# Kernel tuning notes

Measured on AMD Instinct MI355X. Metric: run time of the kernel, lower is better.

## Reference

```python
import jax, jax.numpy as jnp
import numpy as np

EPS = 1e-6  # flax GroupNorm default


def group_norm(x, scale, bias, num_groups):
    B, H, W, C = x.shape
    xg = x.reshape(B, H, W, num_groups, C // num_groups)
    mean = jnp.mean(xg, axis=(1, 2, 4), keepdims=True)
    var = jnp.var(xg, axis=(1, 2, 4), keepdims=True)
    xg = (xg - mean) * jax.lax.rsqrt(var + EPS)
    return xg.reshape(B, H, W, C) * scale + bias


def nin(h, w, b):
    # 1x1 conv / per-pixel dense: bhwc,cd->bhwd
    return jnp.einsum('bhwc,cd->bhwd', h, w) + b


def setup_inputs() -> dict:
    key = jax.random.key(0)
    ks = jax.random.split(key, 8)
    B, H, W, C = 16, 64, 64, 128
    s = 1.0 / np.sqrt(C)
    return {
        'x': jax.random.normal(ks[0], (B, H, W, C), jnp.float32),
        'gn_scale': jnp.ones((C,), jnp.float32),
        'gn_bias': jnp.zeros((C,), jnp.float32),
        'wq': jax.random.normal(ks[1], (C, C), jnp.float32) * s,
        'bq': jnp.zeros((C,), jnp.float32),
        'wk': jax.random.normal(ks[2], (C, C), jnp.float32) * s,
        'bk': jnp.zeros((C,), jnp.float32),
        'wv': jax.random.normal(ks[3], (C, C), jnp.float32) * s,
        'bv': jnp.zeros((C,), jnp.float32),
        'wo': jax.random.normal(ks[4], (C, C), jnp.float32) * s,
        'bo': jnp.zeros((C,), jnp.float32),
    }


def reference(x, gn_scale, gn_bias, wq, bq, wk, bk, wv, bv, wo, bo):
    B, H, W, C = x.shape
    num_groups = min(C // 4, 32)
    h = group_norm(x, gn_scale, gn_bias, num_groups)
    q = nin(h, wq, bq)
    k = nin(h, wk, bk)
    v = nin(h, wv, bv)
    # dense spatial attention; logits (B,H,W,H*W) materialized as in original
    w = jnp.einsum('bhwc,bHWc->bhwHW', q, k) * (C ** -0.5)
    w = w.reshape(B, H, W, H * W)
    w = jax.nn.softmax(w, axis=-1)
    w = w.reshape(B, H, W, H, W)
    h = jnp.einsum('bhwHW,bHWc->bhwc', w, v)
    h = nin(h, wo, bo)
    return x + h  # skip_rescale=False
```

## Files before the change

### kernel.cpp

```cpp
#include <hip/hip_runtime.h>
#include <hip/hip_bf16.h>

typedef unsigned short ushort_t;
typedef unsigned int uint_t;
typedef __attribute__((ext_vector_type(8))) short bf16x8;
typedef __attribute__((ext_vector_type(4))) float f32x4;

#define MFMA32(a, b, c) __builtin_amdgcn_mfma_f32_16x16x32_bf16(a, b, c, 0, 0, 0)

static constexpr int BATCH = 16;
static constexpr int SEQ   = 4096;
static constexpr int CH    = 128;
static constexpr int NGRP  = 32;
static constexpr float EPS = 1e-6f;
static constexpr float C2 = 0.08838834764831845f * 1.4426950408889634f;

__device__ inline ushort_t f2bf(float f) {
    uint_t u = __float_as_uint(f);
    u = (u + 0x7fff + ((u >> 16) & 1)) >> 16;
    return (ushort_t)u;
}

__device__ inline float exp2_fast(float x) {
    return __builtin_amdgcn_exp2f(x);
}

__global__ __launch_bounds__(256) void gn_wprep(const float* __restrict__ x,
                                                float* __restrict__ stats,
                                                const float* __restrict__ W0,
                                                const float* __restrict__ W1,
                                                const float* __restrict__ W2,
                                                const float* __restrict__ W3,
                                                ushort_t* __restrict__ wt) {
    int bid = blockIdx.x;
    int t = threadIdx.x;
    if (bid >= 256) {
        int m = bid - 256;
        const float* Ws[4] = {W0, W1, W2, W3};
        const float* W = Ws[m];
        ushort_t* out = wt + (size_t)m * CH * CH;
        __shared__ ushort_t tile[128][130];
        for (int i = 0; i < 16; ++i) {
            int idx = (t + i * 256) * 4;
            int kk = idx >> 7, n = idx & 127;
            float4 w4 = *(const float4*)(W + (size_t)kk * CH + n);
            tile[n + 0][kk] = f2bf(w4.x);
            tile[n + 1][kk] = f2bf(w4.y);
            tile[n + 2][kk] = f2bf(w4.z);
            tile[n + 3][kk] = f2bf(w4.w);
        }
        __syncthreads();
        for (int i = 0; i < 8; ++i) {
            int idx = (t + i * 256) * 8;
            int n = idx >> 7, kk = idx & 127;
            ushort_t tmp[8];
            for (int u = 0; u < 8; ++u) tmp[u] = tile[n][kk + u];
            *(uint4*)&out[(size_t)n * CH + kk] = *(const uint4*)tmp;
        }
        return;
    }
    int b = bid >> 4, chunk = bid & 15;
    int c4 = (t & 31) * 4;
    int rowoff = t >> 5;
    const float* xb = x + (size_t)b * SEQ * CH;
    float s1 = 0.f, s2 = 0.f;
    int base_row = chunk * 256;
    for (int i = 0; i < 32; ++i) {
        int r = base_row + i * 8 + rowoff;
        float4 v = *(const float4*)(xb + (size_t)r * CH + c4);
        s1 += v.x + v.y + v.z + v.w;
        s2 += v.x * v.x + v.y * v.y + v.z * v.z + v.w * v.w;
    }
    __shared__ float red[256][2];
    red[t][0] = s1; red[t][1] = s2;
    __syncthreads();
    if (t < 32) {
        float a1 = 0.f, a2 = 0.f;
        for (int ro = 0; ro < 8; ++ro) {
            a1 += red[ro * 32 + t][0];
            a2 += red[ro * 32 + t][1];
        }
        float* slot = stats + ((size_t)(b * 16 + chunk) * 32 + t) * 2;
        slot[0] = a1;
        slot[1] = a2;
    }
}

__global__ __launch_bounds__(512) void gemm_qkv(const float* __restrict__ x,
                                                const float* __restrict__ stats,
                                                const float* __restrict__ gsc,
                                                const float* __restrict__ gbi,
                                                const ushort_t* __restrict__ wt,
                                                const float* __restrict__ Bq,
                                                const float* __restrict__ Bk,
                                                const float* __restrict__ Bv,
                                                ushort_t* __restrict__ outq,
                                                ushort_t* __restrict__ outk,
                                                ushort_t* __restrict__ outvt) {
    __shared__ ushort_t lds_a[128][136];
    __shared__ float2 gstat[32];
    int t = threadIdx.x;
    int wv = t >> 6, lane = t & 63, quad = lane >> 4, l16 = lane & 15;
    size_t m0 = (size_t)blockIdx.x * 128;
    int batch = (int)(m0 >> 12);
    int seq0  = (int)(m0 & 4095);
    if (t < 32) {
        float sum = 0.f, sq = 0.f;
        for (int c = 0; c < 16; ++c) {
            const float* slot = stats + ((size_t)(batch * 16 + c) * 32 + t) * 2;
            sum += slot[0];
            sq  += slot[1];
        }
        float mean = sum / 16384.f;
        float var  = sq / 16384.f - mean * mean;
        gstat[t] = float2{mean, __frsqrt_rn(var + EPS)};
    }
    __syncthreads();
    for (int i = 0; i < 4; ++i) {
        int idx = (t + i * 512) * 8;
        int r = idx >> 7, c = idx & 127;
        size_t row = m0 + r;
        float4 xa = *(const float4*)(x + row * CH + c);
        float4 xc = *(const float4*)(x + row * CH + c + 4);
        float2 stA = gstat[c >> 2];
        float2 stB = gstat[(c >> 2) + 1];
        float4 sA = *(const float4*)(gsc + c), sB = *(const float4*)(gsc + c + 4);
        float4 bA = *(const float4*)(gbi + c), bB = *(const float4*)(gbi + c + 4);
        ushort_t tmp[8];
        tmp[0] = f2bf((xa.x - stA.x) * stA.y * sA.x + bA.x);
        tmp[1] = f2bf((xa.y - stA.x) * stA.y * sA.y + bA.y);
        tmp[2] = f2bf((xa.z - stA.x) * stA.y * sA.z + bA.z);
        tmp[3] = f2bf((xa.w - stA.x) * stA.y * sA.w + bA.w);
        tmp[4] = f2bf((xc.x - stB.x) * stB.y * sB.x + bB.x);
        tmp[5] = f2bf((xc.y - stB.x) * stB.y * sB.y + bB.y);
        tmp[6] = f2bf((xc.z - stB.x) * stB.y * sB.z + bB.z);
        tmp[7] = f2bf((xc.w - stB.x) * stB.y * sB.w + bB.w);
        *(uint4*)&lds_a[r][c] = *(const uint4*)tmp;
    }
    __syncthreads();
    for (int j = 0; j < 3; ++j) {
        const ushort_t* wtj = wt + (size_t)j * CH * CH;
        const float* Bi = (j == 0) ? Bq : (j == 1) ? Bk : Bv;
        f32x4 acc[8] = {};
        for (int kh = 0; kh < 2; ++kh) {
            int k0 = kh * 64;
            for (int ks = 0; ks < 2; ++ks) {
                bf16x8 afrag = *(const bf16x8*)&lds_a[wv * 16 + l16][k0 + ks * 32 + quad * 8];
                for (int tc = 0; tc < 8; ++tc) {
                    bf16x8 bfrag = *(const bf16x8*)(wtj + (size_t)(tc * 16 + l16) * CH + k0 + ks * 32 + quad * 8);
                    acc[tc] = MFMA32(afrag, bfrag, acc[tc]);
                }
            }
        }
        int rl = wv * 16 + quad * 4;
        for (int tc = 0; tc < 8; ++tc) {
            int col = tc * 16 + l16;
            float bval = Bi[col];
            if (j == 2) {
                ushort_t tmp[4];
                for (int r = 0; r < 4; ++r) tmp[r] = f2bf(acc[tc][r] + bval);
                *(uint2*)&outvt[(size_t)batch * CH * SEQ + (size_t)col * SEQ + seq0 + rl] =
                    *(const uint2*)tmp;
            } else {
                ushort_t* op = (j == 0) ? outq : outk;
                for (int r = 0; r < 4; ++r) {
                    float vv = acc[tc][r] + bval;
                    if (j == 0) vv *= C2;
                    op[(m0 + rl + r) * CH + col] = f2bf(vv);
                }
            }
        }
    }
}

__global__ __launch_bounds__(256, 2) void flash_attn18(const ushort_t* __restrict__ q,
                                                       const ushort_t* __restrict__ k,
                                                       const ushort_t* __restrict__ vt,
                                                       ushort_t* __restrict__ o) {
    int bid = blockIdx.x;
    int b = bid & 15, qt = bid >> 4;
    int t = threadIdx.x;
    int wv = t >> 6, lane = t & 63, quad = lane >> 4, l16 = lane & 15;
    const size_t SB = (size_t)SEQ * CH;
    const ushort_t* qb  = q  + (size_t)b * SB;
    const ushort_t* kb  = k  + (size_t)b * SB;
    const ushort_t* vtb = vt + (size_t)b * SB;

    __shared__ ushort_t lds_k[2][64][136];
    __shared__ ushort_t lds_vt[2][128][72];

    int qrow_base = qt * 128 + wv * 32;
    bf16x8 qfrag[2][4];
#pragma unroll
    for (int nt = 0; nt < 2; ++nt)
#pragma unroll
        for (int ks = 0; ks < 4; ++ks)
            qfrag[nt][ks] = *(const bf16x8*)(qb + (size_t)(qrow_base + nt * 16 + l16) * CH + ks * 32 + quad * 8);

    f32x4 oacc[8][2] = {};
    float psum[2] = {0.f, 0.f};

    int kr_row  = t >> 4;
    int kr_col  = (t & 15) * 8;
    int vr_d    = t >> 3;
    int vr_beta = t & 7;
    int vc0 = 32 * (vr_beta >> 2) + 16 * (vr_beta & 1) + 4 * ((vr_beta >> 1) & 1);

    const ushort_t* kp = kb + (size_t)kr_row * CH + kr_col;
    const ushort_t* vp = vtb + (size_t)vr_d * SEQ + vr_beta * 8;

    uint4 kr[4], vr[4], k1[4];
#pragma unroll
    for (int i = 0; i < 4; ++i) kr[i] = *(const uint4*)(kp + (size_t)i * 16 * CH);
#pragma unroll
    for (int i = 0; i < 4; ++i) vr[i] = *(const uint4*)(vp + (size_t)i * 32 * SEQ);
#pragma unroll
    for (int i = 0; i < 4; ++i) k1[i] = *(const uint4*)(kp + (size_t)(64 + i * 16) * CH);
    kp += 2 * 64 * CH;
    vp += 64;
#pragma unroll
    for (int i = 0; i < 4; ++i) {
        *(uint4*)&lds_k[0][kr_row + 16 * i][kr_col] = kr[i];
        *(uint4*)&lds_k[1][kr_row + 16 * i][kr_col] = k1[i];
        *(uint2*)&lds_vt[0][vr_d + 32 * i][vc0]     = uint2{vr[i].x, vr[i].y};
        *(uint2*)&lds_vt[0][vr_d + 32 * i][vc0 + 8] = uint2{vr[i].z, vr[i].w};
    }
    __syncthreads();

    bf16x8 pkp[2][2];
    {
        f32x4 s[4][2] = {};
#pragma unroll
        for (int ks = 0; ks < 4; ++ks) {
            bf16x8 kf[4];
#pragma unroll
            for (int kt = 0; kt < 4; ++kt)
                kf[kt] = *(const bf16x8*)&lds_k[0][kt * 16 + l16][ks * 32 + quad * 8];
#pragma unroll
            for (int kt = 0; kt < 4; ++kt) {
                s[kt][0] = MFMA32(kf[kt], qfrag[0][ks], s[kt][0]);
                s[kt][1] = MFMA32(kf[kt], qfrag[1][ks], s[kt][1]);
            }
        }
#pragma unroll
        for (int nt = 0; nt < 2; ++nt) {
            float ps = 0.f;
            uint_t pb[8];
#pragma unroll
            for (int kt = 0; kt < 4; ++kt) {
                float p0 = exp2_fast(s[kt][nt][0]);
                float p1 = exp2_fast(s[kt][nt][1]);
                float p2 = exp2_fast(s[kt][nt][2]);
                float p3 = exp2_fast(s[kt][nt][3]);
                ps += (p0 + p1) + (p2 + p3);
                __hip_bfloat162 h01 = __float22bfloat162_rn(float2{p0, p1});
                __hip_bfloat162 h23 = __float22bfloat162_rn(float2{p2, p3});
                __builtin_memcpy(&pb[kt * 2 + 0], &h01, 4);
                __builtin_memcpy(&pb[kt * 2 + 1], &h23, 4);
            }
            psum[nt] += ps;
            __builtin_memcpy(&pkp[nt][0], &pb[0], 16);
            __builtin_memcpy(&pkp[nt][1], &pb[4], 16);
        }
    }
    __syncthreads();

    for (int it = 0; it < 63; ++it) {
        int knxt = (it + 1) & 1;
        int vcur = it & 1;
#pragma unroll
        for (int i = 0; i < 4; ++i) kr[i] = *(const uint4*)(kp + (size_t)i * 16 * CH);
#pragma unroll
        for (int i = 0; i < 4; ++i) vr[i] = *(const uint4*)(vp + (size_t)i * 32 * SEQ);
        kp += 64 * CH; vp += 64;

        f32x4 s[4][2] = {};
#pragma unroll
        for (int u = 0; u < 4; ++u) {
            bf16x8 kf[4];
#pragma unroll
            for (int kt = 0; kt < 4; ++kt)
                kf[kt] = *(const bf16x8*)&lds_k[knxt][kt * 16 + l16][u * 32 + quad * 8];
#pragma unroll
            for (int kt = 0; kt < 4; ++kt) {
                s[kt][0] = MFMA32(kf[kt], qfrag[0][u], s[kt][0]);
                s[kt][1] = MFMA32(kf[kt], qfrag[1][u], s[kt][1]);
            }
#pragma unroll
            for (int m2 = 0; m2 < 2; ++m2) {
                int mt = u * 2 + m2;
                bf16x8 vf0 = *(const bf16x8*)&lds_vt[vcur][mt * 16 + l16][quad * 8];
                bf16x8 vf1 = *(const bf16x8*)&lds_vt[vcur][mt * 16 + l16][32 + quad * 8];
                oacc[mt][0] = MFMA32(vf0, pkp[0][0], oacc[mt][0]);
                oacc[mt][0] = MFMA32(vf1, pkp[0][1], oacc[mt][0]);
                oacc[mt][1] = MFMA32(vf0, pkp[1][0], oacc[mt][1]);
                oacc[mt][1] = MFMA32(vf1, pkp[1][1], oacc[mt][1]);
            }
        }

#pragma unroll
        for (int nt = 0; nt < 2; ++nt) {
            float ps = 0.f;
            uint_t pb[8];
#pragma unroll
            for (int kt = 0; kt < 4; ++kt) {
                float p0 = exp2_fast(s[kt][nt][0]);
                float p1 = exp2_fast(s[kt][nt][1]);
                float p2 = exp2_fast(s[kt][nt][2]);
                float p3 = exp2_fast(s[kt][nt][3]);
                ps += (p0 + p1) + (p2 + p3);
                __hip_bfloat162 h01 = __float22bfloat162_rn(float2{p0, p1});
                __hip_bfloat162 h23 = __float22bfloat162_rn(float2{p2, p3});
                __builtin_memcpy(&pb[kt * 2 + 0], &h01, 4);
                __builtin_memcpy(&pb[kt * 2 + 1], &h23, 4);
            }
            psum[nt] += ps;
            __builtin_memcpy(&pkp[nt][0], &pb[0], 16);
            __builtin_memcpy(&pkp[nt][1], &pb[4], 16);
        }

#pragma unroll
        for (int i = 0; i < 4; ++i) {
            *(uint4*)&lds_k[vcur][kr_row + 16 * i][kr_col] = kr[i];
            *(uint2*)&lds_vt[knxt][vr_d + 32 * i][vc0]     = uint2{vr[i].x, vr[i].y};
            *(uint2*)&lds_vt[knxt][vr_d + 32 * i][vc0 + 8] = uint2{vr[i].z, vr[i].w};
        }
        __syncthreads();
    }

#pragma unroll
    for (int mt = 0; mt < 8; ++mt) {
        bf16x8 vf0 = *(const bf16x8*)&lds_vt[1][mt * 16 + l16][quad * 8];
        bf16x8 vf1 = *(const bf16x8*)&lds_vt[1][mt * 16 + l16][32 + quad * 8];
        oacc[mt][0] = MFMA32(vf0, pkp[0][0], oacc[mt][0]);
        oacc[mt][0] = MFMA32(vf1, pkp[0][1], oacc[mt][0]);
        oacc[mt][1] = MFMA32(vf0, pkp[1][0], oacc[mt][1]);
        oacc[mt][1] = MFMA32(vf1, pkp[1][1], oacc[mt][1]);
    }

#pragma unroll
    for (int nt = 0; nt < 2; ++nt) {
        float tot = psum[nt];
        tot += __shfl_xor(tot, 16, 64);
        tot += __shfl_xor(tot, 32, 64);
        float inv = 1.f / tot;
        size_t row = (size_t)b * SEQ + qrow_base + nt * 16 + l16;
#pragma unroll
        for (int mt = 0; mt < 8; ++mt) {
            ushort_t tmp[4];
#pragma unroll
            for (int r = 0; r < 4; ++r) tmp[r] = f2bf(oacc[mt][nt][r] * inv);
            *(uint2*)&o[row * CH + mt * 16 + quad * 4] = *(const uint2*)tmp;
        }
    }
}

__global__ __launch_bounds__(512) void gemm_out(const ushort_t* __restrict__ A,
                                                const ushort_t* __restrict__ wto,
                                                const float* __restrict__ bias,
                                                const float* __restrict__ resid,
                                                float* __restrict__ out) {
    __shared__ ushort_t lds_a[128][136];
    int t = threadIdx.x;
    int wv = t >> 6, lane = t & 63, quad = lane >> 4, l16 = lane & 15;
    size_t m0 = (size_t)blockIdx.x * 128;
    for (int i = 0; i < 4; ++i) {
        int idx = (t + i * 512) * 8;
        int r = idx >> 7, c = idx & 127;
        *(uint4*)&lds_a[r][c] = *(const uint4*)(A + (m0 + r) * CH + c);
    }
    __syncthreads();
    f32x4 acc[8] = {};
    for (int kh = 0; kh < 2; ++kh) {
        int k0 = kh * 64;
        for (int ks = 0; ks < 2; ++ks) {
            bf16x8 afrag = *(const bf16x8*)&lds_a[wv * 16 + l16][k0 + ks * 32 + quad * 8];
            for (int tc = 0; tc < 8; ++tc) {
                bf16x8 bfrag = *(const bf16x8*)(wto + (size_t)(tc * 16 + l16) * CH + k0 + ks * 32 + quad * 8);
                acc[tc] = MFMA32(afrag, bfrag, acc[tc]);
            }
        }
    }
    int rl = wv * 16 + quad * 4;
    for (int tc = 0; tc < 8; ++tc) {
        int col = tc * 16 + l16;
        float bval = bias[col];
        for (int r = 0; r < 4; ++r) {
            size_t row = m0 + rl + r;
            out[row * CH + col] = acc[tc][r] + bval + resid[row * CH + col];
        }
    }
}

extern "C" void kernel_launch(void* const* d_in, const int* in_sizes, int n_in,
                              void* d_out, int out_size, void* d_ws, size_t ws_size,
                              hipStream_t stream) {
    const float* x   = (const float*)d_in[0];
    const float* gsc = (const float*)d_in[1];
    const float* gbi = (const float*)d_in[2];
    const float* wq  = (const float*)d_in[3];
    const float* bq  = (const float*)d_in[4];
    const float* wk  = (const float*)d_in[5];
    const float* bk  = (const float*)d_in[6];
    const float* wvp = (const float*)d_in[7];
    const float* bv  = (const float*)d_in[8];
    const float* wo  = (const float*)d_in[9];
    const float* bo  = (const float*)d_in[10];
    float* outp = (float*)d_out;

    const size_t NELEM = (size_t)BATCH * SEQ * CH;
    ushort_t* qbuf  = (ushort_t*)d_ws;
    ushort_t* kbuf  = qbuf + NELEM;
    ushort_t* vtbuf = kbuf + NELEM;
    ushort_t* abuf  = vtbuf + NELEM;
    ushort_t* wtbuf = abuf + NELEM;
    float*    stats = (float*)(wtbuf + 4 * CH * CH);

    gn_wprep<<<260, 256, 0, stream>>>(x, stats, wq, wk, wvp, wo, wtbuf);
    gemm_qkv<<<512, 512, 0, stream>>>(x, stats, gsc, gbi, wtbuf, bq, bk, bv,
                                      qbuf, kbuf, vtbuf);
    flash_attn18<<<512, 256, 0, stream>>>(qbuf, kbuf, vtbuf, abuf);
    gemm_out<<<512, 512, 0, stream>>>(abuf, wtbuf + 3 * CH * CH, bo, x, outp);
}
```

Baseline: 302.8 us.

## Fuse output projection into attention epilogue and double rows per wave in QKV GEMM

Result: faster. 278.5 us (-8.0%).

```diff
diff --git a/kernel.cpp b/kernel.cpp
--- a/kernel.cpp
+++ b/kernel.cpp
@@ -86,7 +86,7 @@
     }
 }
 
-__global__ __launch_bounds__(512) void gemm_qkv(const float* __restrict__ x,
+__global__ __launch_bounds__(256) void gemm_qkv(const float* __restrict__ x,
                                                 const float* __restrict__ stats,
                                                 const float* __restrict__ gsc,
                                                 const float* __restrict__ gbi,
@@ -116,8 +116,8 @@
         gstat[t] = float2{mean, __frsqrt_rn(var + EPS)};
     }
     __syncthreads();
-    for (int i = 0; i < 4; ++i) {
-        int idx = (t + i * 512) * 8;
+    for (int i = 0; i < 8; ++i) {
+        int idx = (t + i * 256) * 8;
         int r = idx >> 7, c = idx & 127;
         size_t row = m0 + r;
         float4 xa = *(const float4*)(x + row * CH + c);
@@ -141,42 +141,50 @@
     for (int j = 0; j < 3; ++j) {
         const ushort_t* wtj = wt + (size_t)j * CH * CH;
         const float* Bi = (j == 0) ? Bq : (j == 1) ? Bk : Bv;
-        f32x4 acc[8] = {};
+        f32x4 acc[2][8] = {};
         for (int kh = 0; kh < 2; ++kh) {
             int k0 = kh * 64;
             for (int ks = 0; ks < 2; ++ks) {
-                bf16x8 afrag = *(const bf16x8*)&lds_a[wv * 16 + l16][k0 + ks * 32 + quad * 8];
+                bf16x8 afrag[2];
+                for (int tr = 0; tr < 2; ++tr)
+                    afrag[tr] = *(const bf16x8*)&lds_a[wv * 32 + tr * 16 + l16][k0 + ks * 32 + quad * 8];
                 for (int tc = 0; tc < 8; ++tc) {
                     bf16x8 bfrag = *(const bf16x8*)(wtj + (size_t)(tc * 16 + l16) * CH + k0 + ks * 32 + quad * 8);
-                    acc[tc] = MFMA32(afrag, bfrag, acc[tc]);
+                    for (int tr = 0; tr < 2; ++tr)
+                        acc[tr][tc] = MFMA32(afrag[tr], bfrag, acc[tr][tc]);
                 }
             }
         }
-        int rl = wv * 16 + quad * 4;
         for (int tc = 0; tc < 8; ++tc) {
             int col = tc * 16 + l16;
             float bval = Bi[col];
-            if (j == 2) {
-                ushort_t tmp[4];
-                for (int r = 0; r < 4; ++r) tmp[r] = f2bf(acc[tc][r] + bval);
-                *(uint2*)&outvt[(size_t)batch * CH * SEQ + (size_t)col * SEQ + seq0 + rl] =
-                    *(const uint2*)tmp;
-            } else {
-                ushort_t* op = (j == 0) ? outq : outk;
-                for (int r = 0; r < 4; ++r) {
-                    float vv = acc[tc][r] + bval;
-                    if (j == 0) vv *= C2;
-                    op[(m0 + rl + r) * CH + col] = f2bf(vv);
+            for (int tr = 0; tr < 2; ++tr) {
+                int rl = wv * 32 + tr * 16 + quad * 4;
+                if (j == 2) {
+                    ushort_t tmp[4];
+                    for (int r = 0; r < 4; ++r) tmp[r] = f2bf(acc[tr][tc][r] + bval);
+                    *(uint2*)&outvt[(size_t)batch * CH * SEQ + (size_t)col * SEQ + seq0 + rl] =
+                        *(const uint2*)tmp;
+                } else {
+                    ushort_t* op = (j == 0) ? outq : outk;
+                    for (int r = 0; r < 4; ++r) {
+                        float vv = acc[tr][tc][r] + bval;
+                        if (j == 0) vv *= C2;
+                        op[(m0 + rl + r) * CH + col] = f2bf(vv);
+                    }
                 }
             }
         }
     }
 }
 
-__global__ __launch_bounds__(256, 2) void flash_attn18(const ushort_t* __restrict__ q,
+__global__ __launch_bounds__(256, 2) void flash_attn21(const ushort_t* __restrict__ q,
                                                        const ushort_t* __restrict__ k,
                                                        const ushort_t* __restrict__ vt,
-                                                       ushort_t* __restrict__ o) {
+                                                       const ushort_t* __restrict__ wto,
+                                                       const float* __restrict__ Bo,
+                                                       const float* __restrict__ xres,
+                                                       float* __restrict__ outp) {
     int bid = blockIdx.x;
     int b = bid & 15, qt = bid >> 4;
     int t = threadIdx.x;
@@ -338,56 +346,49 @@
         oacc[mt][1] = MFMA32(vf1, pkp[1][1], oacc[mt][1]);
     }
 
+    float inv_[2];
 #pragma unroll
     for (int nt = 0; nt < 2; ++nt) {
         float tot = psum[nt];
         tot += __shfl_xor(tot, 16, 64);
         tot += __shfl_xor(tot, 32, 64);
-        float inv = 1.f / tot;
-        size_t row = (size_t)b * SEQ + qrow_base + nt * 16 + l16;
+        inv_[nt] = 1.f / tot;
+    }
+
+    __syncthreads();
+    ushort_t* slice = ((ushort_t*)lds_k) + (size_t)wv * 32 * 136;
+#pragma unroll
+    for (int nt = 0; nt < 2; ++nt) {
 #pragma unroll
         for (int mt = 0; mt < 8; ++mt) {
             ushort_t tmp[4];
 #pragma unroll
-            for (int r = 0; r < 4; ++r) tmp[r] = f2bf(oacc[mt][nt][r] * inv);
-            *(uint2*)&o[row * CH + mt * 16 + quad * 4] = *(const uint2*)tmp;
-        }
-    }
-}
-
-__global__ __launch_bounds__(512) void gemm_out(const ushort_t* __restrict__ A,
-                                                const ushort_t* __restrict__ wto,
-                                                const float* __restrict__ bias,
-                                                const float* __restrict__ resid,
-                                                float* __restrict__ out) {
-    __shared__ ushort_t lds_a[128][136];
-    int t = threadIdx.x;
-    int wv = t >> 6, lane = t & 63, quad = lane >> 4, l16 = lane & 15;
-    size_t m0 = (size_t)blockIdx.x * 128;
-    for (int i = 0; i < 4; ++i) {
-        int idx = (t + i * 512) * 8;
-        int r = idx >> 7, c = idx & 127;
-        *(uint4*)&lds_a[r][c] = *(const uint4*)(A + (m0 + r) * CH + c);
-    }
-    __syncthreads();
-    f32x4 acc[8] = {};
-    for (int kh = 0; kh < 2; ++kh) {
-        int k0 = kh * 64;
-        for (int ks = 0; ks < 2; ++ks) {
-            bf16x8 afrag = *(const bf16x8*)&lds_a[wv * 16 + l16][k0 + ks * 32 + quad * 8];
+            for (int r = 0; r < 4; ++r) tmp[r] = f2bf(oacc[mt][nt][r] * inv_[nt]);
+            *(uint2*)&slice[(nt * 16 + l16) * 136 + mt * 16 + quad * 4] = *(const uint2*)tmp;
+        }
+    }
+#pragma unroll
+    for (int nt = 0; nt < 2; ++nt) {
+        f32x4 acc2[8] = {};
+#pragma unroll
+        for (int ks2 = 0; ks2 < 4; ++ks2) {
+            bf16x8 afrag = *(const bf16x8*)&slice[(nt * 16 + l16) * 136 + ks2 * 32 + quad * 8];
+#pragma unroll
             for (int tc = 0; tc < 8; ++tc) {
-                bf16x8 bfrag = *(const bf16x8*)(wto + (size_t)(tc * 16 + l16) * CH + k0 + ks * 32 + quad * 8);
-                acc[tc] = MFMA32(afrag, bfrag, acc[tc]);
-            }
-        }
-    }
-    int rl = wv * 16 + quad * 4;
-    for (int tc = 0; tc < 8; ++tc) {
-        int col = tc * 16 + l16;
-        float bval = bias[col];
-        for (int r = 0; r < 4; ++r) {
-            size_t row = m0 + rl + r;
-            out[row * CH + col] = acc[tc][r] + bval + resid[row * CH + col];
+                bf16x8 bfrag = *(const bf16x8*)(wto + (size_t)(tc * 16 + l16) * CH + ks2 * 32 + quad * 8);
+                acc2[tc] = MFMA32(afrag, bfrag, acc2[tc]);
+            }
+        }
+        size_t rowbase = (size_t)b * SEQ + qrow_base + nt * 16 + quad * 4;
+#pragma unroll
+        for (int tc = 0; tc < 8; ++tc) {
+            int col = tc * 16 + l16;
+            float bval = Bo[col];
+#pragma unroll
+            for (int r = 0; r < 4; ++r) {
+                size_t row = rowbase + r;
+                outp[row * CH + col] = acc2[tc][r] + bval + xres[row * CH + col];
+            }
         }
     }
 }
@@ -412,13 +413,12 @@
     ushort_t* qbuf  = (ushort_t*)d_ws;
     ushort_t* kbuf  = qbuf + NELEM;
     ushort_t* vtbuf = kbuf + NELEM;
-    ushort_t* abuf  = vtbuf + NELEM;
-    ushort_t* wtbuf = abuf + NELEM;
+    ushort_t* wtbuf = vtbuf + NELEM;
     float*    stats = (float*)(wtbuf + 4 * CH * CH);
 
     gn_wprep<<<260, 256, 0, stream>>>(x, stats, wq, wk, wvp, wo, wtbuf);
-    gemm_qkv<<<512, 512, 0, stream>>>(x, stats, gsc, gbi, wtbuf, bq, bk, bv,
+    gemm_qkv<<<512, 256, 0, stream>>>(x, stats, gsc, gbi, wtbuf, bq, bk, bv,
                                       qbuf, kbuf, vtbuf);
-    flash_attn18<<<512, 256, 0, stream>>>(qbuf, kbuf, vtbuf, abuf);
-    gemm_out<<<512, 512, 0, stream>>>(abuf, wtbuf + 3 * CH * CH, bo, x, outp);
-}
+    flash_attn21<<<512, 256, 0, stream>>>(qbuf, kbuf, vtbuf,
+                                          wtbuf + 3 * CH * CH, bo, x, outp);
+}
```
